# Kernel tuning notes

Hardware: AMD Instinct MI355X
Metric: run time of the kernel (lower is better)

The kernel has to match this reference:

```python
import jax, jax.numpy as jnp
import numpy as np
from jax import lax

N, D = 32768, 512
N_Q, BINS = 8, 2048


def setup_inputs() -> dict:
    key = jax.random.key(0)
    k1, k2 = jax.random.split(key)
    hidden_states = jax.random.normal(k1, (N, D), dtype=jnp.float32)
    # learned codebooks: n_q stages, each [BINS, D] (bins list clamps to one size)
    codebooks = jax.random.normal(k2, (N_Q, BINS, D), dtype=jnp.float32)
    return {"hidden_states": hidden_states, "codebooks": codebooks}


def reference(hidden_states, codebooks):
    """ResidualVectorQuantizer.encode: sequential residual VQ over n_q codebooks.

    Distances sum((r - c)^2) computed via the GEMM expansion
    ||r||^2 - 2 r.c^T + ||c||^2 (same math, matmul-friendly).
    Returns (codes [n_q, N] int, quantized [N, D]).
    """
    cb_sq = jnp.sum(codebooks * codebooks, axis=-1)  # [n_q, bins]

    def step(carry, stage):
        residual, quantized = carry
        cb, csq = stage  # [bins, D], [bins]
        r_sq = jnp.sum(residual * residual, axis=-1, keepdims=True)  # [N, 1]
        dist = r_sq - 2.0 * (residual @ cb.T) + csq[None, :]  # [N, bins]
        idx = jnp.argmin(dist, axis=-1)  # [N]
        chosen = cb[idx]  # [N, D]
        return (residual - chosen, quantized + chosen), idx

    init = (hidden_states, jnp.zeros_like(hidden_states))
    (_, quantized), codes = lax.scan(step, init, (codebooks, cb_sq))
    return codes, quantized
```

## Files before the change

### kernel.cpp

```cpp
#include <hip/hip_runtime.h>
#include <hip/hip_bf16.h>

#define NROWS 32768
#define DIM   512
#define NQ    8
#define NBINS 2048

#define MARGIN 1.0f

typedef __attribute__((ext_vector_type(8))) short short8v;
typedef __attribute__((ext_vector_type(4))) float f32x4;

__device__ inline unsigned short f2bf(float x) {
    __hip_bfloat16 h = __float2bfloat16(x);
    return *reinterpret_cast<unsigned short*>(&h);
}

typedef __attribute__((address_space(3))) void lds_t;
typedef __attribute__((address_space(1))) const void gbl_t;
__device__ inline void gload16(const void* g, void* l) {
    __builtin_amdgcn_global_load_lds((gbl_t*)g, (lds_t*)l, 16, 0, 0);
}

__device__ inline float pw_combine(float s) {
#pragma unroll
    for (int m = 1; m <= 16; m <<= 1) {
        float o = __shfl_xor(s, m, 64);
        s = __fadd_rn(s, o);
    }
    return s;
}

__global__ __launch_bounds__(256) void k_prep(const float* __restrict__ cb,
                                              unsigned short* __restrict__ o,
                                              float* __restrict__ csq32) {
    int row = blockIdx.x * 4 + (threadIdx.x >> 6);
    int lane = threadIdx.x & 63;
    const float* cp = cb + (size_t)row * DIM;

    float4 a = *(const float4*)(cp + lane * 8);
    float4 b = *(const float4*)(cp + lane * 8 + 4);
    short8v v;
    v[0] = f2bf(a.x); v[1] = f2bf(a.y); v[2] = f2bf(a.z); v[3] = f2bf(a.w);
    v[4] = f2bf(b.x); v[5] = f2bf(b.y); v[6] = f2bf(b.z); v[7] = f2bf(b.w);
    *(short8v*)(o + (size_t)row * DIM + lane * 8) = v;

    float s = 0.0f;
    if (lane < 32) {
        int base = (lane >> 3) * 128 + (lane & 7);
        float e = cp[base];
        s = __fmul_rn(e, e);
#pragma unroll
        for (int m = 1; m < 16; ++m) {
            float e2 = cp[base + 8 * m];
            s = __fadd_rn(s, __fmul_rn(e2, e2));
        }
    }
    s = pw_combine(s);
    if (lane == 0) csq32[row] = s;
}

__global__ __launch_bounds__(128) void k_init(const float* __restrict__ h,
                                              float* __restrict__ rout,
                                              float* __restrict__ rsq,
                                              unsigned short* __restrict__ ahi) {
    int row = blockIdx.x;
    int t = threadIdx.x;
    __shared__ float sq[DIM];
    float4 r = *(const float4*)(h + (size_t)row * DIM + t * 4);
    *(float4*)(rout + (size_t)row * DIM + t * 4) = r;
    ushort4 hv;
    hv.x = f2bf(r.x); hv.y = f2bf(r.y); hv.z = f2bf(r.z); hv.w = f2bf(r.w);
    *(ushort4*)(ahi + (size_t)row * DIM + t * 4) = hv;
    sq[t * 4 + 0] = __fmul_rn(r.x, r.x);
    sq[t * 4 + 1] = __fmul_rn(r.y, r.y);
    sq[t * 4 + 2] = __fmul_rn(r.z, r.z);
    sq[t * 4 + 3] = __fmul_rn(r.w, r.w);
    __syncthreads();
    if (t < 32) {
        int base = (t >> 3) * 128 + (t & 7);
        float s = sq[base];
#pragma unroll
        for (int m = 1; m < 16; ++m) s = __fadd_rn(s, sq[base + 8 * m]);
        s = pw_combine(s);
        if (t == 0) rsq[row] = s;
    }
}

__global__ __launch_bounds__(256, 4) void k_gemm(const unsigned short* __restrict__ Ahi,
                                                 const unsigned short* __restrict__ Bcb,
                                                 const float* __restrict__ csq,
                                                 float* __restrict__ partD,
                                                 int* __restrict__ partI) {
    __shared__ __align__(16) char lds[33792];
    __shared__ float csqS[128];

    const int tid = threadIdx.x;
    const int lane = tid & 63;
    const int w = tid >> 6;
    const int wr = w >> 1;
    const int wc = w & 1;

    const int wg = blockIdx.x;
    const int seq = wg >> 3;
    const int panel = (wg & 7) * 32 + (seq >> 8) * 16 + (seq & 15);
    const int T = (seq >> 4) & 15;

    if (tid < 128) csqS[tid] = csq[T * 128 + tid];

    const char* Abase = (const char*)(Ahi + (size_t)panel * 128 * DIM);
    const char* Bbase = (const char*)(Bcb + (size_t)T * 128 * DIM);

    int goff[4], loff[4];
#pragma unroll
    for (int i = 0; i < 4; ++i) {
        int L = i * 256 + tid;
        int row = L >> 3, cc = L & 7;
        goff[i] = row * (DIM * 2) + ((cc ^ (row & 7)) << 4);
        loff[i] = L * 16;
    }

    f32x4 acc[4][4];
#pragma unroll
    for (int m = 0; m < 4; ++m)
#pragma unroll
        for (int n = 0; n < 4; ++n) acc[m][n] = (f32x4){0.f, 0.f, 0.f, 0.f};

#pragma unroll
    for (int ks = 0; ks < 8; ++ks) {
        __syncthreads();
        const int k0b = ks * 128;
#pragma unroll
        for (int i = 0; i < 4; ++i) {
            gload16(Abase + goff[i] + k0b, lds + loff[i]);
            gload16(Bbase + goff[i] + k0b, lds + 16384 + loff[i]);
        }
        __syncthreads();
        __builtin_amdgcn_s_setprio(1);
        const char* Ab = lds;
        const char* Bb = lds + 16384;
#pragma unroll
        for (int kk = 0; kk < 2; ++kk) {
            const int sw = (((kk * 4 + (lane >> 4)) ^ (lane & 7)) << 4);
            short8v bF[4];
#pragma unroll
            for (int n = 0; n < 4; ++n) {
                int rowB = wc * 64 + n * 16 + (lane & 15);
                bF[n] = *(const short8v*)(Bb + rowB * 128 + sw);
            }
#pragma unroll
            for (int m = 0; m < 4; ++m) {
                int rowA = wr * 64 + m * 16 + (lane & 15);
                short8v aF = *(const short8v*)(Ab + rowA * 128 + sw);
#pragma unroll
                for (int n = 0; n < 4; ++n)
                    acc[m][n] = __builtin_amdgcn_mfma_f32_16x16x32_bf16(
                        aF, bF[n], acc[m][n], 0, 0, 0);
            }
        }
        __builtin_amdgcn_s_setprio(0);
    }

    float td0 = 3.4e38f, td1 = 3.4e38f, td2 = 3.4e38f, td3 = 3.4e38f;
    int ti0 = 0, ti1 = 0, ti2 = 0, ti3 = 0;
    float* distf = (float*)lds;
    const int row2 = tid >> 1, h = tid & 1;

#pragma unroll
    for (int p = 0; p < 2; ++p) {
        __syncthreads();
        if (wc == p) {
#pragma unroll
            for (int m = 0; m < 4; ++m)
#pragma unroll
                for (int n = 0; n < 4; ++n)
#pragma unroll
                    for (int r = 0; r < 4; ++r) {
                        int row = wr * 64 + m * 16 + (lane >> 4) * 4 + r;
                        int cl = n * 16 + (lane & 15);
                        distf[row * 66 + cl] = csqS[p * 64 + cl] - 2.0f * acc[m][n][r];
                    }
        }
        __syncthreads();
        int binb = T * 128 + p * 64 + h * 32;
        for (int c = 0; c < 32; ++c) {
            float d = distf[row2 * 66 + h * 32 + c];
            int bin = binb + c;
            if (d < td3) {
                if (d < td2) {
                    td3 = td2; ti3 = ti2;
                    if (d < td1) {
                        td2 = td1; ti2 = ti1;
                        if (d < td0) { td1 = td0; ti1 = ti0; td0 = d; ti0 = bin; }
                        else { td1 = d; ti1 = bin; }
                    } else { td2 = d; ti2 = bin; }
                } else { td3 = d; ti3 = bin; }
            }
        }
    }
#pragma unroll
    for (int j = 0; j < 4; ++j) {
        float d = __shfl_xor(j == 0 ? td0 : (j == 1 ? td1 : (j == 2 ? td2 : td3)), 1);
        int bin = __shfl_xor(j == 0 ? ti0 : (j == 1 ? ti1 : (j == 2 ? ti2 : ti3)), 1);
        if (d < td3) {
            if (d < td2) {
                td3 = td2; ti3 = ti2;
                if (d < td1) {
                    td2 = td1; ti2 = ti1;
                    if (d < td0) { td1 = td0; ti1 = ti0; td0 = d; ti0 = bin; }
                    else { td1 = d; ti1 = bin; }
                } else { td2 = d; ti2 = bin; }
            } else { td3 = d; ti3 = bin; }
        }
    }
    if (h == 0) {
        size_t g = ((size_t)panel * 128 + row2) * 64 + T * 4;
        partD[g + 0] = td0; partI[g + 0] = ti0;
        partD[g + 1] = td1; partI[g + 1] = ti1;
        partD[g + 2] = td2; partI[g + 2] = ti2;
        partD[g + 3] = td3; partI[g + 3] = ti3;
    }
}

__global__ __launch_bounds__(256) void k_ru(const float* __restrict__ partD,
                                            const int* __restrict__ partI,
                                            float* __restrict__ resid,
                                            float* __restrict__ rsq,
                                            const float* __restrict__ csq,
                                            const float* __restrict__ cb,
                                            float* __restrict__ codeOut,
                                            unsigned short* __restrict__ ahi,
                                            const float* __restrict__ hidden,
                                            int last) {
    const int w = threadIdx.x >> 6;
    const int lane = threadIdx.x & 63;
    const int row = blockIdx.x * 4 + w;
    __shared__ float sq[4][DIM];

    const float* rp = resid + (size_t)row * DIM;
    float4 r0 = *(const float4*)(rp + lane * 8);
    float4 r1 = *(const float4*)(rp + lane * 8 + 4);

    float d = partD[(size_t)row * 64 + lane];
    int bi0 = partI[(size_t)row * 64 + lane];
    float bd = d; int bix = bi0;
#pragma unroll
    for (int o = 32; o > 0; o >>= 1) {
        float od = __shfl_xor(bd, o);
        int oi = __shfl_xor(bix, o);
        if (od < bd || (od == bd && oi < bix)) { bd = od; bix = oi; }
    }
    bool cand = (d <= bd + MARGIN);
    unsigned long long mask = __ballot(cand);
    int winI;
    if (__popcll(mask) == 1) {
        winI = bix;
    } else {
        float myD = 3.4e38f; int myI = 0x7fffffff;
        if (cand) {
            const float* cp = cb + (size_t)bi0 * DIM;
            float acc = 0.0f;
            for (int k = 0; k < DIM; k += 4) {
                float4 rv = *(const float4*)(rp + k);
                float4 cv = *(const float4*)(cp + k);
                acc = fmaf(rv.x, cv.x, acc);
                acc = fmaf(rv.y, cv.y, acc);
                acc = fmaf(rv.z, cv.z, acc);
                acc = fmaf(rv.w, cv.w, acc);
            }
            myD = __fadd_rn(__fsub_rn(rsq[row], __fmul_rn(2.0f, acc)), csq[bi0]);
            myI = bi0;
        }
#pragma unroll
        for (int o = 32; o > 0; o >>= 1) {
            float od = __shfl_xor(myD, o);
            int oi = __shfl_xor(myI, o);
            if (od < myD || (od == myD && oi < myI)) { myD = od; myI = oi; }
        }
        winI = myI;
    }
    if (lane == 0) codeOut[row] = (float)winI;
    const int id = winI;

    const float* cp8 = cb + (size_t)id * DIM + lane * 8;
    float4 c0 = *(const float4*)cp8;
    float4 c1 = *(const float4*)(cp8 + 4);
    r0.x = __fsub_rn(r0.x, c0.x);
    r0.y = __fsub_rn(r0.y, c0.y);
    r0.z = __fsub_rn(r0.z, c0.z);
    r0.w = __fsub_rn(r0.w, c0.w);
    r1.x = __fsub_rn(r1.x, c1.x);
    r1.y = __fsub_rn(r1.y, c1.y);
    r1.z = __fsub_rn(r1.z, c1.z);
    r1.w = __fsub_rn(r1.w, c1.w);

    float* wp = resid + (size_t)row * DIM + lane * 8;
    if (last) {
        const float* hp = hidden + (size_t)row * DIM + lane * 8;
        float4 h0 = *(const float4*)hp;
        float4 h1 = *(const float4*)(hp + 4);
        float4 q0, q1;
        q0.x = __fsub_rn(h0.x, r0.x);
        q0.y = __fsub_rn(h0.y, r0.y);
        q0.z = __fsub_rn(h0.z, r0.z);
        q0.w = __fsub_rn(h0.w, r0.w);
        q1.x = __fsub_rn(h1.x, r1.x);
        q1.y = __fsub_rn(h1.y, r1.y);
        q1.z = __fsub_rn(h1.z, r1.z);
        q1.w = __fsub_rn(h1.w, r1.w);
        *(float4*)wp = q0;
        *(float4*)(wp + 4) = q1;
        return;
    }

    *(float4*)wp = r0;
    *(float4*)(wp + 4) = r1;
    short8v hv;
    hv[0] = f2bf(r0.x); hv[1] = f2bf(r0.y); hv[2] = f2bf(r0.z); hv[3] = f2bf(r0.w);
    hv[4] = f2bf(r1.x); hv[5] = f2bf(r1.y); hv[6] = f2bf(r1.z); hv[7] = f2bf(r1.w);
    *(short8v*)(ahi + (size_t)row * DIM + lane * 8) = hv;

    sq[w][lane * 8 + 0] = __fmul_rn(r0.x, r0.x);
    sq[w][lane * 8 + 1] = __fmul_rn(r0.y, r0.y);
    sq[w][lane * 8 + 2] = __fmul_rn(r0.z, r0.z);
    sq[w][lane * 8 + 3] = __fmul_rn(r0.w, r0.w);
    sq[w][lane * 8 + 4] = __fmul_rn(r1.x, r1.x);
    sq[w][lane * 8 + 5] = __fmul_rn(r1.y, r1.y);
    sq[w][lane * 8 + 6] = __fmul_rn(r1.z, r1.z);
    sq[w][lane * 8 + 7] = __fmul_rn(r1.w, r1.w);
    __syncthreads();
    if (lane < 32) {
        int base = (lane >> 3) * 128 + (lane & 7);
        float s = sq[w][base];
#pragma unroll
        for (int m = 1; m < 16; ++m) s = __fadd_rn(s, sq[w][base + 8 * m]);
        s = pw_combine(s);
        if (lane == 0) rsq[row] = s;
    }
}

extern "C" void kernel_launch(void* const* d_in, const int* in_sizes, int n_in,
                              void* d_out, int out_size, void* d_ws, size_t ws_size,
                              hipStream_t stream) {
    const float* hidden = (const float*)d_in[0];
    const float* cbs = (const float*)d_in[1];

    float* out_codes = (float*)d_out;
    float* resid = out_codes + (size_t)NQ * NROWS;

    unsigned short* Ahi = (unsigned short*)d_ws;
    unsigned short* Cbf = Ahi + (size_t)NROWS * DIM;
    float* csq32 = (float*)(Cbf + (size_t)NQ * NBINS * DIM);
    float* rsq = csq32 + (size_t)NQ * NBINS;
    float* partD = rsq + NROWS;
    int* partI = (int*)(partD + (size_t)NROWS * 64);

    k_prep<<<NQ * NBINS / 4, 256, 0, stream>>>(cbs, Cbf, csq32);
    k_init<<<NROWS, 128, 0, stream>>>(hidden, resid, rsq, Ahi);

    for (int s = 0; s < NQ; ++s) {
        const float* cbS = cbs + (size_t)s * NBINS * DIM;
        k_gemm<<<(NROWS / 128) * (NBINS / 128), 256, 0, stream>>>(
            Ahi, Cbf + (size_t)s * NBINS * DIM, csq32 + (size_t)s * NBINS,
            partD, partI);
        k_ru<<<NROWS / 4, 256, 0, stream>>>(partD, partI, resid, rsq,
                                            csq32 + (size_t)s * NBINS, cbS,
                                            out_codes + (size_t)s * NROWS, Ahi,
                                            hidden, s == NQ - 1);
    }
}
```

Before: 1.243 ms.

## Switch distance GEMM from bf16 to int8 MFMA with per-row scales

Residuals and codebook rows are quantized to int8 with per-row absmax scales, and the distance GEMM uses the i32 16x16x64 int8 MFMA instead of bf16. Distances are rescaled in the epilogue, and the candidate margin grows from 1 to 8 so the exact top-4 refinement can absorb the coarser approximation. This halves GEMM operand bytes and uses higher-throughput int8 matrix instructions. The risks are a weaker candidate ranking, and that the fixed margin may not always contain the true argmin. The init kernel also moves to four rows per block.

```diff
diff --git a/kernel.cpp b/kernel.cpp
--- a/kernel.cpp
+++ b/kernel.cpp
@@ -6,15 +6,10 @@
 #define NQ    8
 #define NBINS 2048
 
-#define MARGIN 1.0f
-
-typedef __attribute__((ext_vector_type(8))) short short8v;
+#define MARGIN 8.0f
+
 typedef __attribute__((ext_vector_type(4))) float f32x4;
-
-__device__ inline unsigned short f2bf(float x) {
-    __hip_bfloat16 h = __float2bfloat16(x);
-    return *reinterpret_cast<unsigned short*>(&h);
-}
+typedef __attribute__((ext_vector_type(4))) int i32x4;
 
 typedef __attribute__((address_space(3))) void lds_t;
 typedef __attribute__((address_space(1))) const void gbl_t;
@@ -31,19 +26,35 @@
     return s;
 }
 
+__device__ inline int q8(float v, float qs) {
+    float x = fminf(fmaxf(v * qs, -127.0f), 127.0f);
+    return __float2int_rn(x) & 255;
+}
+__device__ inline int pack4(float a, float b, float c, float d, float qs) {
+    return q8(a, qs) | (q8(b, qs) << 8) | (q8(c, qs) << 16) | (q8(d, qs) << 24);
+}
+
 __global__ __launch_bounds__(256) void k_prep(const float* __restrict__ cb,
-                                              unsigned short* __restrict__ o,
-                                              float* __restrict__ csq32) {
+                                              unsigned char* __restrict__ o,
+                                              float* __restrict__ csq32,
+                                              float* __restrict__ sclc) {
     int row = blockIdx.x * 4 + (threadIdx.x >> 6);
     int lane = threadIdx.x & 63;
     const float* cp = cb + (size_t)row * DIM;
 
     float4 a = *(const float4*)(cp + lane * 8);
     float4 b = *(const float4*)(cp + lane * 8 + 4);
-    short8v v;
-    v[0] = f2bf(a.x); v[1] = f2bf(a.y); v[2] = f2bf(a.z); v[3] = f2bf(a.w);
-    v[4] = f2bf(b.x); v[5] = f2bf(b.y); v[6] = f2bf(b.z); v[7] = f2bf(b.w);
-    *(short8v*)(o + (size_t)row * DIM + lane * 8) = v;
+
+    float mx = fmaxf(fmaxf(fmaxf(fabsf(a.x), fabsf(a.y)), fmaxf(fabsf(a.z), fabsf(a.w))),
+                     fmaxf(fmaxf(fabsf(b.x), fabsf(b.y)), fmaxf(fabsf(b.z), fabsf(b.w))));
+#pragma unroll
+    for (int m2 = 32; m2 > 0; m2 >>= 1) mx = fmaxf(mx, __shfl_xor(mx, m2));
+    float qs = (mx > 0.0f) ? 127.0f / mx : 0.0f;
+
+    int2 pv;
+    pv.x = pack4(a.x, a.y, a.z, a.w, qs);
+    pv.y = pack4(b.x, b.y, b.z, b.w, qs);
+    *(int2*)(o + (size_t)row * DIM + lane * 8) = pv;
 
     float s = 0.0f;
     if (lane < 32) {
@@ -57,43 +68,68 @@
         }
     }
     s = pw_combine(s);
-    if (lane == 0) csq32[row] = s;
-}
-
-__global__ __launch_bounds__(128) void k_init(const float* __restrict__ h,
+    if (lane == 0) {
+        csq32[row] = s;
+        sclc[row] = (mx > 0.0f) ? mx / 127.0f : 0.0f;
+    }
+}
+
+__global__ __launch_bounds__(256) void k_init(const float* __restrict__ h,
                                               float* __restrict__ rout,
                                               float* __restrict__ rsq,
-                                              unsigned short* __restrict__ ahi) {
-    int row = blockIdx.x;
-    int t = threadIdx.x;
-    __shared__ float sq[DIM];
-    float4 r = *(const float4*)(h + (size_t)row * DIM + t * 4);
-    *(float4*)(rout + (size_t)row * DIM + t * 4) = r;
-    ushort4 hv;
-    hv.x = f2bf(r.x); hv.y = f2bf(r.y); hv.z = f2bf(r.z); hv.w = f2bf(r.w);
-    *(ushort4*)(ahi + (size_t)row * DIM + t * 4) = hv;
-    sq[t * 4 + 0] = __fmul_rn(r.x, r.x);
-    sq[t * 4 + 1] = __fmul_rn(r.y, r.y);
-    sq[t * 4 + 2] = __fmul_rn(r.z, r.z);
-    sq[t * 4 + 3] = __fmul_rn(r.w, r.w);
+                                              unsigned char* __restrict__ a8,
+                                              float* __restrict__ sclr) {
+    int row = blockIdx.x * 4 + (threadIdx.x >> 6);
+    int w = threadIdx.x >> 6;
+    int lane = threadIdx.x & 63;
+    __shared__ float sq[4][DIM];
+
+    const float* hp = h + (size_t)row * DIM + lane * 8;
+    float4 r0 = *(const float4*)hp;
+    float4 r1 = *(const float4*)(hp + 4);
+    float* wp = rout + (size_t)row * DIM + lane * 8;
+    *(float4*)wp = r0;
+    *(float4*)(wp + 4) = r1;
+
+    float mx = fmaxf(fmaxf(fmaxf(fabsf(r0.x), fabsf(r0.y)), fmaxf(fabsf(r0.z), fabsf(r0.w))),
+                     fmaxf(fmaxf(fabsf(r1.x), fabsf(r1.y)), fmaxf(fabsf(r1.z), fabsf(r1.w))));
+#pragma unroll
+    for (int m2 = 32; m2 > 0; m2 >>= 1) mx = fmaxf(mx, __shfl_xor(mx, m2));
+    float qs = (mx > 0.0f) ? 127.0f / mx : 0.0f;
+    int2 pv;
+    pv.x = pack4(r0.x, r0.y, r0.z, r0.w, qs);
+    pv.y = pack4(r1.x, r1.y, r1.z, r1.w, qs);
+    *(int2*)(a8 + (size_t)row * DIM + lane * 8) = pv;
+    if (lane == 0) sclr[row] = (mx > 0.0f) ? mx / 127.0f : 0.0f;
+
+    sq[w][lane * 8 + 0] = __fmul_rn(r0.x, r0.x);
+    sq[w][lane * 8 + 1] = __fmul_rn(r0.y, r0.y);
+    sq[w][lane * 8 + 2] = __fmul_rn(r0.z, r0.z);
+    sq[w][lane * 8 + 3] = __fmul_rn(r0.w, r0.w);
+    sq[w][lane * 8 + 4] = __fmul_rn(r1.x, r1.x);
+    sq[w][lane * 8 + 5] = __fmul_rn(r1.y, r1.y);
+    sq[w][lane * 8 + 6] = __fmul_rn(r1.z, r1.z);
+    sq[w][lane * 8 + 7] = __fmul_rn(r1.w, r1.w);
     __syncthreads();
-    if (t < 32) {
-        int base = (t >> 3) * 128 + (t & 7);
-        float s = sq[base];
-#pragma unroll
-        for (int m = 1; m < 16; ++m) s = __fadd_rn(s, sq[base + 8 * m]);
+    if (lane < 32) {
+        int base = (lane >> 3) * 128 + (lane & 7);
+        float s = sq[w][base];
+#pragma unroll
+        for (int m = 1; m < 16; ++m) s = __fadd_rn(s, sq[w][base + 8 * m]);
         s = pw_combine(s);
-        if (t == 0) rsq[row] = s;
-    }
-}
-
-__global__ __launch_bounds__(256, 4) void k_gemm(const unsigned short* __restrict__ Ahi,
-                                                 const unsigned short* __restrict__ Bcb,
+        if (lane == 0) rsq[row] = s;
+    }
+}
+
+__global__ __launch_bounds__(256, 4) void k_gemm(const unsigned char* __restrict__ A8,
+                                                 const unsigned char* __restrict__ B8,
                                                  const float* __restrict__ csq,
+                                                 const float* __restrict__ sclr,
+                                                 const float* __restrict__ sclc,
                                                  float* __restrict__ partD,
                                                  int* __restrict__ partI) {
     __shared__ __align__(16) char lds[33792];
-    __shared__ float csqS[128];
+    __shared__ float csqS[128], sclcS[128], sclrS[128];
 
     const int tid = threadIdx.x;
     const int lane = tid & 63;
@@ -106,57 +142,57 @@
     const int panel = (wg & 7) * 32 + (seq >> 8) * 16 + (seq & 15);
     const int T = (seq >> 4) & 15;
 
-    if (tid < 128) csqS[tid] = csq[T * 128 + tid];
-
-    const char* Abase = (const char*)(Ahi + (size_t)panel * 128 * DIM);
-    const char* Bbase = (const char*)(Bcb + (size_t)T * 128 * DIM);
-
-    int goff[4], loff[4];
-#pragma unroll
-    for (int i = 0; i < 4; ++i) {
+    if (tid < 128) {
+        csqS[tid] = csq[T * 128 + tid];
+        sclcS[tid] = sclc[T * 128 + tid];
+        sclrS[tid] = sclr[panel * 128 + tid];
+    }
+
+    const char* Abase = (const char*)(A8 + (size_t)panel * 128 * DIM);
+    const char* Bbase = (const char*)(B8 + (size_t)T * 128 * DIM);
+
+    int goff[2], loff[2];
+#pragma unroll
+    for (int i = 0; i < 2; ++i) {
         int L = i * 256 + tid;
-        int row = L >> 3, cc = L & 7;
-        goff[i] = row * (DIM * 2) + ((cc ^ (row & 7)) << 4);
+        int row = L >> 2, cc = L & 3;
+        goff[i] = row * DIM + ((cc ^ ((row >> 1) & 3)) << 4);
         loff[i] = L * 16;
     }
 
-    f32x4 acc[4][4];
+    i32x4 acc[4][4];
 #pragma unroll
     for (int m = 0; m < 4; ++m)
 #pragma unroll
-        for (int n = 0; n < 4; ++n) acc[m][n] = (f32x4){0.f, 0.f, 0.f, 0.f};
+        for (int n = 0; n < 4; ++n) acc[m][n] = (i32x4){0, 0, 0, 0};
+
+    const int arow = lane & 15;
+    const int slot = ((lane >> 4) ^ ((arow >> 1) & 3)) << 4;
 
 #pragma unroll
     for (int ks = 0; ks < 8; ++ks) {
         __syncthreads();
-        const int k0b = ks * 128;
-#pragma unroll
-        for (int i = 0; i < 4; ++i) {
+        const int k0b = ks * 64;
+#pragma unroll
+        for (int i = 0; i < 2; ++i) {
             gload16(Abase + goff[i] + k0b, lds + loff[i]);
-            gload16(Bbase + goff[i] + k0b, lds + 16384 + loff[i]);
+            gload16(Bbase + goff[i] + k0b, lds + 8192 + loff[i]);
         }
         __syncthreads();
         __builtin_amdgcn_s_setprio(1);
         const char* Ab = lds;
-        const char* Bb = lds + 16384;
-#pragma unroll
-        for (int kk = 0; kk < 2; ++kk) {
-            const int sw = (((kk * 4 + (lane >> 4)) ^ (lane & 7)) << 4);
-            short8v bF[4];
-#pragma unroll
-            for (int n = 0; n < 4; ++n) {
-                int rowB = wc * 64 + n * 16 + (lane & 15);
-                bF[n] = *(const short8v*)(Bb + rowB * 128 + sw);
-            }
-#pragma unroll
-            for (int m = 0; m < 4; ++m) {
-                int rowA = wr * 64 + m * 16 + (lane & 15);
-                short8v aF = *(const short8v*)(Ab + rowA * 128 + sw);
-#pragma unroll
-                for (int n = 0; n < 4; ++n)
-                    acc[m][n] = __builtin_amdgcn_mfma_f32_16x16x32_bf16(
-                        aF, bF[n], acc[m][n], 0, 0, 0);
-            }
+        const char* Bb = lds + 8192;
+        i32x4 bF[4];
+#pragma unroll
+        for (int n = 0; n < 4; ++n)
+            bF[n] = *(const i32x4*)(Bb + (wc * 64 + n * 16 + arow) * 64 + slot);
+#pragma unroll
+        for (int m = 0; m < 4; ++m) {
+            i32x4 aF = *(const i32x4*)(Ab + (wr * 64 + m * 16 + arow) * 64 + slot);
+#pragma unroll
+            for (int n = 0; n < 4; ++n)
+                acc[m][n] = __builtin_amdgcn_mfma_i32_16x16x64_i8(
+                    aF, bF[n], acc[m][n], 0, 0, 0);
         }
         __builtin_amdgcn_s_setprio(0);
     }
@@ -178,7 +214,8 @@
                     for (int r = 0; r < 4; ++r) {
                         int row = wr * 64 + m * 16 + (lane >> 4) * 4 + r;
                         int cl = n * 16 + (lane & 15);
-                        distf[row * 66 + cl] = csqS[p * 64 + cl] - 2.0f * acc[m][n][r];
+                        float dq = 2.0f * sclrS[row] * sclcS[p * 64 + cl];
+                        distf[row * 66 + cl] = csqS[p * 64 + cl] - (float)acc[m][n][r] * dq;
                     }
         }
         __syncthreads();
@@ -229,7 +266,8 @@
                                             const float* __restrict__ csq,
                                             const float* __restrict__ cb,
                                             float* __restrict__ codeOut,
-                                            unsigned short* __restrict__ ahi,
+                                            unsigned char* __restrict__ a8,
+                                            float* __restrict__ sclr,
                                             const float* __restrict__ hidden,
                                             int last) {
     const int w = threadIdx.x >> 6;
@@ -315,10 +353,17 @@
 
     *(float4*)wp = r0;
     *(float4*)(wp + 4) = r1;
-    short8v hv;
-    hv[0] = f2bf(r0.x); hv[1] = f2bf(r0.y); hv[2] = f2bf(r0.z); hv[3] = f2bf(r0.w);
-    hv[4] = f2bf(r1.x); hv[5] = f2bf(r1.y); hv[6] = f2bf(r1.z); hv[7] = f2bf(r1.w);
-    *(short8v*)(ahi + (size_t)row * DIM + lane * 8) = hv;
+
+    float mx = fmaxf(fmaxf(fmaxf(fabsf(r0.x), fabsf(r0.y)), fmaxf(fabsf(r0.z), fabsf(r0.w))),
+                     fmaxf(fmaxf(fabsf(r1.x), fabsf(r1.y)), fmaxf(fabsf(r1.z), fabsf(r1.w))));
+#pragma unroll
+    for (int m2 = 32; m2 > 0; m2 >>= 1) mx = fmaxf(mx, __shfl_xor(mx, m2));
+    float qs = (mx > 0.0f) ? 127.0f / mx : 0.0f;
+    int2 pv;
+    pv.x = pack4(r0.x, r0.y, r0.z, r0.w, qs);
+    pv.y = pack4(r1.x, r1.y, r1.z, r1.w, qs);
+    *(int2*)(a8 + (size_t)row * DIM + lane * 8) = pv;
+    if (lane == 0) sclr[row] = (mx > 0.0f) ? mx / 127.0f : 0.0f;
 
     sq[w][lane * 8 + 0] = __fmul_rn(r0.x, r0.x);
     sq[w][lane * 8 + 1] = __fmul_rn(r0.y, r0.y);
@@ -348,24 +393,26 @@
     float* out_codes = (float*)d_out;
     float* resid = out_codes + (size_t)NQ * NROWS;
 
-    unsigned short* Ahi = (unsigned short*)d_ws;
-    unsigned short* Cbf = Ahi + (size_t)NROWS * DIM;
-    float* csq32 = (float*)(Cbf + (size_t)NQ * NBINS * DIM);
-    float* rsq = csq32 + (size_t)NQ * NBINS;
+    unsigned char* A8 = (unsigned char*)d_ws;
+    unsigned char* Cb8 = A8 + (size_t)NROWS * DIM;
+    float* csq32 = (float*)(Cb8 + (size_t)NQ * NBINS * DIM);
+    float* sclc = csq32 + (size_t)NQ * NBINS;
+    float* sclr = sclc + (size_t)NQ * NBINS;
+    float* rsq = sclr + NROWS;
     float* partD = rsq + NROWS;
     int* partI = (int*)(partD + (size_t)NROWS * 64);
 
-    k_prep<<<NQ * NBINS / 4, 256, 0, stream>>>(cbs, Cbf, csq32);
-    k_init<<<NROWS, 128, 0, stream>>>(hidden, resid, rsq, Ahi);
+    k_prep<<<NQ * NBINS / 4, 256, 0, stream>>>(cbs, Cb8, csq32, sclc);
+    k_init<<<NROWS / 4, 256, 0, stream>>>(hidden, resid, rsq, A8, sclr);
 
     for (int s = 0; s < NQ; ++s) {
         const float* cbS = cbs + (size_t)s * NBINS * DIM;
         k_gemm<<<(NROWS / 128) * (NBINS / 128), 256, 0, stream>>>(
-            Ahi, Cbf + (size_t)s * NBINS * DIM, csq32 + (size_t)s * NBINS,
-            partD, partI);
+            A8, Cb8 + (size_t)s * NBINS * DIM, csq32 + (size_t)s * NBINS,
+            sclr, sclc + (size_t)s * NBINS, partD, partI);
         k_ru<<<NROWS / 4, 256, 0, stream>>>(partD, partI, resid, rsq,
                                             csq32 + (size_t)s * NBINS, cbS,
-                                            out_codes + (size_t)s * NROWS, Ahi,
+                                            out_codes + (size_t)s * NROWS, A8, sclr,
                                             hidden, s == NQ - 1);
     }
 }
```

After: 1.535 ms. +23.4%, slower.
